# Kernel optimization log

Hardware: AMD Instinct MI355X
Metric: run time of the kernel (lower is better)

Reference implementation:

```python
import jax, jax.numpy as jnp
import numpy as np

NUM_ITER = 3
SLOT_DIM = 16
INPUT_DIM = 256
HIDDEN_DIM = 128
EPS = 1e-8
LN_EPS = 1e-5  # torch LayerNorm default


def _layernorm(x, w, b):
    mu = jnp.mean(x, axis=-1, keepdims=True)
    var = jnp.mean((x - mu) ** 2, axis=-1, keepdims=True)
    return (x - mu) * jax.lax.rsqrt(var + LN_EPS) * w + b


def setup_inputs() -> dict:
    key = jax.random.key(0)
    ks = jax.random.split(key, 12)
    B, N, K = 32, 4096, 8
    D, S, H = INPUT_DIM, SLOT_DIM, HIDDEN_DIM
    inputs = jax.random.normal(ks[0], (B, N, D), dtype=jnp.float32)
    init_slots = jax.random.normal(ks[1], (B, K, S), dtype=jnp.float32)
    return {
        "inputs": inputs,
        "init_slots": init_slots,
        "ln_in_w": jnp.ones((D,), jnp.float32),
        "ln_in_b": jnp.zeros((D,), jnp.float32),
        "ln_s_w": jnp.ones((S,), jnp.float32),
        "ln_s_b": jnp.zeros((S,), jnp.float32),
        "ln_m_w": jnp.ones((S,), jnp.float32),
        "ln_m_b": jnp.zeros((S,), jnp.float32),
        "wq": jax.random.normal(ks[2], (S, S), jnp.float32) * (S ** -0.5),
        "wk": jax.random.normal(ks[3], (S, D), jnp.float32) * (D ** -0.5),
        "wv": jax.random.normal(ks[4], (S, D), jnp.float32) * (D ** -0.5),
        "w_ih": jax.random.normal(ks[5], (3 * S, S), jnp.float32) * (S ** -0.5),
        "w_hh": jax.random.normal(ks[6], (3 * S, S), jnp.float32) * (S ** -0.5),
        "b_ih": jnp.zeros((3 * S,), jnp.float32),
        "b_hh": jnp.zeros((3 * S,), jnp.float32),
        "mlp_w1": jax.random.normal(ks[7], (H, S), jnp.float32) * (S ** -0.5),
        "mlp_b1": jnp.zeros((H,), jnp.float32),
        "mlp_w2": jax.random.normal(ks[8], (S, H), jnp.float32) * (H ** -0.5),
        "mlp_b2": jnp.zeros((S,), jnp.float32),
    }


def _gru_cell(x, h, w_ih, w_hh, b_ih, b_hh):
    # torch GRUCell: gates ordered [r, z, n]
    gi = x @ w_ih.T + b_ih            # [BK, 3S]
    gh = h @ w_hh.T + b_hh
    i_r, i_z, i_n = jnp.split(gi, 3, axis=-1)
    h_r, h_z, h_n = jnp.split(gh, 3, axis=-1)
    r = jax.nn.sigmoid(i_r + h_r)
    z = jax.nn.sigmoid(i_z + h_z)
    n = jnp.tanh(i_n + r * h_n)
    return (1.0 - z) * n + z * h


def reference(inputs, init_slots, ln_in_w, ln_in_b, ln_s_w, ln_s_b, ln_m_w, ln_m_b,
              wq, wk, wv, w_ih, w_hh, b_ih, b_hh, mlp_w1, mlp_b1, mlp_w2, mlp_b2):
    B, N, _ = inputs.shape
    K = init_slots.shape[1]
    scale = SLOT_DIM ** -0.5

    x = _layernorm(inputs, ln_in_w, ln_in_b)
    k = jnp.einsum('bnd,sd->bns', x, wk)   # [B,N,S]
    v = jnp.einsum('bnd,sd->bns', x, wv)

    slots = init_slots
    attn = None
    for _ in range(NUM_ITER):
        slots_prev = slots
        q = jnp.einsum('bks,ts->bkt', _layernorm(slots, ln_s_w, ln_s_b), wq)
        logits = jnp.einsum('bks,bns->bkn', q, k) * scale       # [B,K,N]
        attn = jax.nn.softmax(logits, axis=1) + EPS              # softmax over SLOTS
        attn = attn / jnp.sum(attn, axis=-1, keepdims=True)
        updates = jnp.einsum('bkn,bns->bks', attn, v)            # [B,K,S]
        h = _gru_cell(updates.reshape(B * K, -1), slots_prev.reshape(B * K, -1),
                      w_ih, w_hh, b_ih, b_hh).reshape(B, K, -1)
        y = _layernorm(h, ln_m_w, ln_m_b)
        mlp = jax.nn.relu(y @ mlp_w1.T + mlp_b1) @ mlp_w2.T + mlp_b2
        slots = h + mlp
    return slots, attn
```

## Files before the change

kernel.cpp:

```cpp
#include <hip/hip_runtime.h>
#include <cstddef>


__device__ __forceinline__ float sigmoid_f(float x){ return 1.f/(1.f+__expf(-x)); }
__device__ __forceinline__ float tanh_f(float x){ return 1.f - 2.f/(__expf(2.f*x)+1.f); }

__device__ __forceinline__ void load16_to_lds(const float* g, float* l) {
  __builtin_amdgcn_global_load_lds(
      (const __attribute__((address_space(1))) unsigned int*)g,
      (__attribute__((address_space(3))) unsigned int*)l,
      16, 0, 0);
}

__global__ __launch_bounds__(256) void k_prep(
    const float* __restrict__ lnw, const float* __restrict__ lnb,
    const float* __restrict__ wk, const float* __restrict__ wv,
    const float* __restrict__ init_slots,
    const float* __restrict__ ln_s_w, const float* __restrict__ ln_s_b,
    const float* __restrict__ wq,
    float* __restrict__ wprepT, float* __restrict__ mt,
    float* __restrict__ qbuf, float* __restrict__ upd, float* __restrict__ Abuf,
    float* __restrict__ slots_out)
{
  int t = threadIdx.x;
  int i = blockIdx.x*256 + t;
  {
    int d64 = i & 63, u = (i >> 6) & 7, p = (i >> 9) & 3, c = i >> 11;
    int s = p*8 + u, d = c*64 + d64;
    float w = (s < 16) ? wk[s*256+d] : wv[(s-16)*256+d];
    wprepT[i] = lnw[d]*w;
  }
  if (blockIdx.x != 0) return;
  {
    int s = t >> 3, j = t & 7;
    float m = 0.f, tv = 0.f;
    for (int d = j; d < 256; d += 8) {
      float w = (s < 16) ? wk[s*256+d] : wv[(s-16)*256+d];
      m  = fmaf(lnw[d], w, m);
      tv = fmaf(lnb[d], w, tv);
    }
    m += __shfl_xor(m,1);  m += __shfl_xor(m,2);  m += __shfl_xor(m,4);
    tv += __shfl_xor(tv,1); tv += __shfl_xor(tv,2); tv += __shfl_xor(tv,4);
    if (j == 0) { mt[s] = m; mt[32+s] = tv; }
  }
  #pragma unroll
  for (int j2 = 0; j2 < 16; ++j2) {
    slots_out[t*16+j2] = init_slots[t*16+j2];
    upd[t*16+j2] = 0.f;
  }
  Abuf[t] = 0.f;
  float sl[16];
  #pragma unroll
  for (int j2 = 0; j2 < 16; ++j2) sl[j2] = init_slots[t*16+j2];
  float mu = 0.f;
  #pragma unroll
  for (int j2 = 0; j2 < 16; ++j2) mu += sl[j2];
  mu *= (1.f/16.f);
  float var = 0.f;
  #pragma unroll
  for (int j2 = 0; j2 < 16; ++j2) { float d = sl[j2]-mu; var = fmaf(d,d,var); }
  var *= (1.f/16.f);
  float rstd = rsqrtf(var + 1e-5f);
  float y[16];
  #pragma unroll
  for (int j2 = 0; j2 < 16; ++j2) y[j2] = (sl[j2]-mu)*rstd*ln_s_w[j2] + ln_s_b[j2];
  #pragma unroll
  for (int tq = 0; tq < 16; ++tq) {
    float q = 0.f;
    #pragma unroll
    for (int s2 = 0; s2 < 16; ++s2) q = fmaf(y[s2], wq[tq*16+s2], q);
    qbuf[t*16+tq] = q;
  }
}

__global__ __launch_bounds__(256, 4) void k_proj(
    const float* __restrict__ x, const float* __restrict__ wprepT,
    const float* __restrict__ mt,
    float* __restrict__ kout, float* __restrict__ vout)
{
  __shared__ float xs[2][64*64];
  int t = threadIdx.x;
  int lane = t & 63;
  int p = __builtin_amdgcn_readfirstlane(t >> 6);
  int r0 = blockIdx.x*64;
  const float* xbase = x + (size_t)r0*256;

  int sr = lane >> 4;
  int slot = lane & 15;
  int row_st0 = p*16 + sr;
  int cb0 = (slot - row_st0) & 15;

  float acc[8];
  #pragma unroll
  for (int u = 0; u < 8; ++u) acc[u] = 0.f;
  float sum = 0.f, sumsq = 0.f;

  #define ISSUE_CHUNK(c_, buf_)                                              \
    _Pragma("unroll")                                                        \
    for (int i = 0; i < 4; ++i) {                                            \
      int row = row_st0 + i*4;                                               \
      int cb  = (cb0 - i*4) & 15;                                            \
      load16_to_lds(xbase + (size_t)row*256 + (c_)*64 + cb*4,                \
                    &xs[buf_][(p*16 + i*4)*64]);                             \
    }

  ISSUE_CHUNK(0, 0)
  __syncthreads();

  #pragma unroll 1
  for (int c = 0; c < 4; ++c) {
    if (c < 3) { ISSUE_CHUNK(c+1, (c+1)&1) }
    const float* wc = wprepT + (c*4 + p)*512;
    const float* xb = xs[c&1];
    #pragma unroll
    for (int g = 0; g < 4; ++g) {
      float xe[16];
      #pragma unroll
      for (int i = 0; i < 4; ++i) {
        int m = g*4 + i;
        float4 f = *(const float4*)&xb[lane*64 + ((m + lane) & 15)*4];
        xe[i*4+0]=f.x; xe[i*4+1]=f.y; xe[i*4+2]=f.z; xe[i*4+3]=f.w;
      }
      #pragma unroll
      for (int j = 0; j < 16; ++j) { sum += xe[j]; sumsq = fmaf(xe[j], xe[j], sumsq); }
      #pragma unroll
      for (int u = 0; u < 8; ++u) {
        const float* w = wc + u*64 + g*16;
        #pragma unroll
        for (int j = 0; j < 16; ++j) acc[u] = fmaf(xe[j], w[j], acc[u]);
      }
    }
    __syncthreads();
  }
  #undef ISSUE_CHUNK

  float mu = sum*(1.f/256.f);
  float var = sumsq*(1.f/256.f) - mu*mu;
  float rstd = rsqrtf(var + 1e-5f);
  float o[8];
  #pragma unroll
  for (int u = 0; u < 8; ++u) {
    int a = p*8 + u;
    o[u] = fmaf(rstd, acc[u] - mu*mt[a], mt[32+a]);
  }
  float* dst = ((p < 2) ? kout : vout) + (size_t)(r0 + lane)*16 + (p & 1)*8;
  *(float4*)(dst+0) = make_float4(o[0],o[1],o[2],o[3]);
  *(float4*)(dst+4) = make_float4(o[4],o[5],o[6],o[7]);
}

__global__ __launch_bounds__(256) void k_attn(
    const float* __restrict__ kproj, const float* __restrict__ vproj,
    const float* __restrict__ qbuf,
    float* __restrict__ upd, float* __restrict__ Abuf,
    float* __restrict__ attn_out, int write_attn)
{
  __shared__ float qs[128];
  __shared__ float ktile[256*20];
  __shared__ float vtile[16*260];
  __shared__ float ptile[8*260];
  int b = blockIdx.x >> 4;
  int n0 = (blockIdx.x & 15) * 256;
  int t = threadIdx.x;

  const float* kbase = kproj + ((size_t)(b*4096 + n0))*16;
  const float* vbase = vproj + ((size_t)(b*4096 + n0))*16;
  {
    int nn = t >> 2, s0 = (t & 3)*4;
    #pragma unroll
    for (int i = 0; i < 4; ++i) {
      int n = i*64 + nn;
      float4 kf = *(const float4*)(kbase + n*16 + s0);
      *(float4*)&ktile[n*20 + s0] = kf;
      float4 vf = *(const float4*)(vbase + n*16 + s0);
      vtile[(s0+0)*260 + n] = vf.x;
      vtile[(s0+1)*260 + n] = vf.y;
      vtile[(s0+2)*260 + n] = vf.z;
      vtile[(s0+3)*260 + n] = vf.w;
    }
  }
  if (t < 128) qs[t] = qbuf[b*128 + t];
  __syncthreads();

  {
    float4 kv[4];
    #pragma unroll
    for (int i = 0; i < 4; ++i) kv[i] = *(const float4*)&ktile[t*20 + i*4];
    const float4* q4 = (const float4*)qs;
    float lg[8];
    #pragma unroll
    for (int kk = 0; kk < 8; ++kk) {
      float4 a4 = make_float4(0.f,0.f,0.f,0.f);
      #pragma unroll
      for (int i = 0; i < 4; ++i) {
        float4 q = q4[kk*4+i];
        a4.x = fmaf(q.x, kv[i].x, a4.x);
        a4.y = fmaf(q.y, kv[i].y, a4.y);
        a4.z = fmaf(q.z, kv[i].z, a4.z);
        a4.w = fmaf(q.w, kv[i].w, a4.w);
      }
      lg[kk] = ((a4.x+a4.y)+(a4.z+a4.w))*0.25f;
    }
    float mx = lg[0];
    #pragma unroll
    for (int kk = 1; kk < 8; ++kk) mx = fmaxf(mx, lg[kk]);
    float se = 0.f;
    #pragma unroll
    for (int kk = 0; kk < 8; ++kk) { lg[kk] = __expf(lg[kk]-mx); se += lg[kk]; }
    float inv = 1.f/se;
    #pragma unroll
    for (int kk = 0; kk < 8; ++kk) {
      float pv = fmaf(lg[kk], inv, 1e-8f);
      ptile[kk*260 + t] = pv;
      if (write_attn) attn_out[((size_t)(b*8+kk))*4096 + n0 + t] = pv;
    }
  }
  __syncthreads();
  {
    int kk = t >> 5, r = t & 31, s = r >> 1, half = r & 1;
    const float4* pr = (const float4*)(ptile + kk*260 + half*128);
    const float4* vr = (const float4*)(vtile + s*260 + half*128);
    float4 a4 = make_float4(0.f,0.f,0.f,0.f);
    float4 s4 = make_float4(0.f,0.f,0.f,0.f);
    #pragma unroll 8
    for (int i = 0; i < 32; ++i) {
      float4 pv = pr[i], vv = vr[i];
      s4.x += pv.x; s4.y += pv.y; s4.z += pv.z; s4.w += pv.w;
      a4.x = fmaf(pv.x, vv.x, a4.x);
      a4.y = fmaf(pv.y, vv.y, a4.y);
      a4.z = fmaf(pv.z, vv.z, a4.z);
      a4.w = fmaf(pv.w, vv.w, a4.w);
    }
    float acc  = (a4.x+a4.y)+(a4.z+a4.w);
    float asum = (s4.x+s4.y)+(s4.z+s4.w);
    acc  += __shfl_xor(acc, 1);
    asum += __shfl_xor(asum, 1);
    if (half == 0) {
      atomicAdd(upd + (b*8+kk)*16 + s, acc);
      if (s == 0) atomicAdd(Abuf + b*8 + kk, asum);
    }
  }
}

__global__ __launch_bounds__(256) void k_gru(
    float* __restrict__ upd, float* __restrict__ Abuf,
    float* __restrict__ slots, float* __restrict__ qbuf,
    const float* __restrict__ w_ih, const float* __restrict__ w_hh,
    const float* __restrict__ b_ih, const float* __restrict__ b_hh,
    const float* __restrict__ mlp_w1, const float* __restrict__ mlp_b1,
    const float* __restrict__ mlp_w2, const float* __restrict__ mlp_b2,
    const float* __restrict__ ln_m_w, const float* __restrict__ ln_m_b,
    const float* __restrict__ ln_s_w, const float* __restrict__ ln_s_b,
    const float* __restrict__ wq, int prep_next)
{
  __shared__ float s_wih[48*17], s_whh[48*17];
  __shared__ float s_bih[48], s_bhh[48];
  __shared__ float s_w1[128*17], s_b1[128];
  __shared__ float s_w2[16*129], s_b2[16];
  __shared__ float s_lnmw[16], s_lnmb[16], s_lnsw[16], s_lnsb[16];
  __shared__ float s_wq[16*17];
  int t = threadIdx.x;
  for (int i = t; i < 768; i += 256) {
    int g = i >> 4, j = i & 15;
    s_wih[g*17+j] = w_ih[i];
    s_whh[g*17+j] = w_hh[i];
  }
  for (int i = t; i < 2048; i += 256) {
    int r = i >> 4, c = i & 15;
    s_w1[r*17+c] = mlp_w1[i];
    int r2 = i >> 7, c2 = i & 127;
    s_w2[r2*129+c2] = mlp_w2[i];
  }
  if (t < 48) { s_bih[t] = b_ih[t]; s_bhh[t] = b_hh[t]; }
  if (t < 128) s_b1[t] = mlp_b1[t];
  if (t < 16) {
    s_b2[t] = mlp_b2[t];
    s_lnmw[t] = ln_m_w[t]; s_lnmb[t] = ln_m_b[t];
    s_lnsw[t] = ln_s_w[t]; s_lnsb[t] = ln_s_b[t];
  }
  for (int i = t; i < 256; i += 256) {
    int r = i >> 4, c = i & 15;
    s_wq[r*17+c] = wq[i];
  }
  __syncthreads();

  int bk = blockIdx.x*16 + (t >> 4);
  int s = t & 15;
  int laneBase = (t & 63) & ~15;

  float inv = 1.f / Abuf[bk];
  float u[16], h[16];
  #pragma unroll
  for (int j = 0; j < 16; ++j) {
    u[j] = upd[bk*16+j] * inv;
    h[j] = slots[bk*16+j];
  }
  float hs = slots[bk*16+s];

  float gir = s_bih[s],  giz = s_bih[16+s], gin = s_bih[32+s];
  float ghr = s_bhh[s],  ghz = s_bhh[16+s], ghn = s_bhh[32+s];
  #pragma unroll
  for (int j = 0; j < 16; ++j) {
    gir = fmaf(u[j], s_wih[s*17+j], gir);
    giz = fmaf(u[j], s_wih[(16+s)*17+j], giz);
    gin = fmaf(u[j], s_wih[(32+s)*17+j], gin);
    ghr = fmaf(h[j], s_whh[s*17+j], ghr);
    ghz = fmaf(h[j], s_whh[(16+s)*17+j], ghz);
    ghn = fmaf(h[j], s_whh[(32+s)*17+j], ghn);
  }
  float rr = sigmoid_f(gir + ghr);
  float zz = sigmoid_f(giz + ghz);
  float nn = tanh_f(gin + rr*ghn);
  float hn = (1.f-zz)*nn + zz*hs;

  float ssum = hn;
  #pragma unroll
  for (int m = 1; m < 16; m <<= 1) ssum += __shfl_xor(ssum, m);
  float mu = ssum*(1.f/16.f);
  float dv = hn - mu;
  float vs = dv*dv;
  #pragma unroll
  for (int m = 1; m < 16; m <<= 1) vs += __shfl_xor(vs, m);
  float rstd = rsqrtf(vs*(1.f/16.f) + 1e-5f);
  float y = dv*rstd*s_lnmw[s] + s_lnmb[s];

  float yv[16];
  #pragma unroll
  for (int j = 0; j < 16; ++j) yv[j] = __shfl(y, laneBase + j);

  float h1[8];
  #pragma unroll
  for (int i = 0; i < 8; ++i) {
    int jj = i*16 + s;
    float a = s_b1[jj];
    #pragma unroll
    for (int q = 0; q < 16; ++q) a = fmaf(yv[q], s_w1[jj*17+q], a);
    h1[i] = fmaxf(a, 0.f);
  }
  float o = s_b2[s];
  #pragma unroll
  for (int i = 0; i < 8; ++i) {
    #pragma unroll
    for (int sp = 0; sp < 16; ++sp) {
      float hv = __shfl(h1[i], laneBase + sp);
      o = fmaf(hv, s_w2[s*129 + i*16 + sp], o);
    }
  }
  float slot_new = hn + o;
  slots[bk*16+s] = slot_new;

  if (prep_next) {
    float ss = slot_new;
    #pragma unroll
    for (int m = 1; m < 16; m <<= 1) ss += __shfl_xor(ss, m);
    float mu2 = ss*(1.f/16.f);
    float d2 = slot_new - mu2;
    float v2 = d2*d2;
    #pragma unroll
    for (int m = 1; m < 16; m <<= 1) v2 += __shfl_xor(v2, m);
    float rstd2 = rsqrtf(v2*(1.f/16.f) + 1e-5f);
    float y2 = d2*rstd2*s_lnsw[s] + s_lnsb[s];
    float qv = 0.f;
    #pragma unroll
    for (int sp = 0; sp < 16; ++sp) qv = fmaf(__shfl(y2, laneBase+sp), s_wq[s*17+sp], qv);
    qbuf[bk*16+s] = qv;
    upd[bk*16+s] = 0.f;
    if (s == 0) Abuf[bk] = 0.f;
  }
}

__global__ __launch_bounds__(256) void k_scale(float* __restrict__ attn,
                                               const float* __restrict__ Abuf)
{
  int bk = blockIdx.x;
  float inv = 1.f / Abuf[bk];
  float4* p = (float4*)(attn + (size_t)bk*4096);
  #pragma unroll 4
  for (int i = threadIdx.x; i < 1024; i += 256) {
    float4 v = p[i];
    v.x *= inv; v.y *= inv; v.z *= inv; v.w *= inv;
    p[i] = v;
  }
}

extern "C" void kernel_launch(void* const* d_in, const int* in_sizes, int n_in,
                              void* d_out, int out_size, void* d_ws, size_t ws_size,
                              hipStream_t stream)
{
  const float* inputs     = (const float*)d_in[0];
  const float* init_slots = (const float*)d_in[1];
  const float* ln_in_w    = (const float*)d_in[2];
  const float* ln_in_b    = (const float*)d_in[3];
  const float* ln_s_w     = (const float*)d_in[4];
  const float* ln_s_b     = (const float*)d_in[5];
  const float* ln_m_w     = (const float*)d_in[6];
  const float* ln_m_b     = (const float*)d_in[7];
  const float* wq         = (const float*)d_in[8];
  const float* wk         = (const float*)d_in[9];
  const float* wv         = (const float*)d_in[10];
  const float* w_ih       = (const float*)d_in[11];
  const float* w_hh       = (const float*)d_in[12];
  const float* b_ih       = (const float*)d_in[13];
  const float* b_hh       = (const float*)d_in[14];
  const float* mlp_w1     = (const float*)d_in[15];
  const float* mlp_b1     = (const float*)d_in[16];
  const float* mlp_w2     = (const float*)d_in[17];
  const float* mlp_b2     = (const float*)d_in[18];

  float* ws    = (float*)d_ws;
  float* wprepT= ws;
  float* mt    = ws + 8192;
  float* qbuf  = ws + 8320;
  float* upd   = ws + 12416;
  float* Abuf  = ws + 16512;
  float* kproj = ws + 16768;
  float* vproj = kproj + 2097152;

  float* out   = (float*)d_out;
  float* slots = out;
  float* attn  = out + 4096;

  k_prep<<<32, 256, 0, stream>>>(ln_in_w, ln_in_b, wk, wv, init_slots,
                                 ln_s_w, ln_s_b, wq,
                                 wprepT, mt, qbuf, upd, Abuf, slots);
  k_proj<<<2048, 256, 0, stream>>>(inputs, wprepT, mt, kproj, vproj);
  for (int it = 0; it < 3; ++it) {
    int last = (it == 2);
    k_attn<<<512, 256, 0, stream>>>(kproj, vproj, qbuf, upd, Abuf, attn, last);
    k_gru<<<16, 256, 0, stream>>>(upd, Abuf, slots, qbuf,
                                  w_ih, w_hh, b_ih, b_hh,
                                  mlp_w1, mlp_b1, mlp_w2, mlp_b2,
                                  ln_m_w, ln_m_b, ln_s_w, ln_s_b,
                                  wq, last ? 0 : 1);
  }
  k_scale<<<256, 256, 0, stream>>>(attn, Abuf);
}
```

Baseline: 338.1 us.

## Compute input K/V projection with split-bf16 MFMA instead of FP32 FMA

The K/V projection kernel now computes on bf16 matrix-core MFMA instructions, using a three-term hi/lo bf16 split of both inputs and weights to approximate FP32 accuracy. Weights are prepped as bf16 hi/lo pairs, and the layernorm mean correction term is adjusted to match the rounded weights. Inputs are read directly from global memory into registers, replacing the LDS double-buffering. This trades scalar FP32 FMA throughput for matrix-core throughput, at the cost of extra conversion work and a small precision loss.

```diff
diff --git a/kernel.cpp b/kernel.cpp
--- a/kernel.cpp
+++ b/kernel.cpp
@@ -2,14 +2,19 @@
 #include <cstddef>
 
 
+typedef unsigned short ushort_t;
+typedef __attribute__((ext_vector_type(8))) short short8;
+typedef __attribute__((ext_vector_type(4))) float f32x4;
+
 __device__ __forceinline__ float sigmoid_f(float x){ return 1.f/(1.f+__expf(-x)); }
 __device__ __forceinline__ float tanh_f(float x){ return 1.f - 2.f/(__expf(2.f*x)+1.f); }
 
-__device__ __forceinline__ void load16_to_lds(const float* g, float* l) {
-  __builtin_amdgcn_global_load_lds(
-      (const __attribute__((address_space(1))) unsigned int*)g,
-      (__attribute__((address_space(3))) unsigned int*)l,
-      16, 0, 0);
+__device__ __forceinline__ ushort_t f2bf(float x){
+  unsigned u = __float_as_uint(x);
+  return (ushort_t)((u + 0x7FFFu + ((u>>16)&1u)) >> 16);
+}
+__device__ __forceinline__ float bf2f(ushort_t b){
+  return __uint_as_float(((unsigned)b) << 16);
 }
 
 __global__ __launch_bounds__(256) void k_prep(
@@ -18,17 +23,20 @@
     const float* __restrict__ init_slots,
     const float* __restrict__ ln_s_w, const float* __restrict__ ln_s_b,
     const float* __restrict__ wq,
-    float* __restrict__ wprepT, float* __restrict__ mt,
+    ushort_t* __restrict__ Wh, ushort_t* __restrict__ Wl,
+    float* __restrict__ mt,
     float* __restrict__ qbuf, float* __restrict__ upd, float* __restrict__ Abuf,
     float* __restrict__ slots_out)
 {
   int t = threadIdx.x;
   int i = blockIdx.x*256 + t;
   {
-    int d64 = i & 63, u = (i >> 6) & 7, p = (i >> 9) & 3, c = i >> 11;
-    int s = p*8 + u, d = c*64 + d64;
+    int s = i >> 8, d = i & 255;
     float w = (s < 16) ? wk[s*256+d] : wv[(s-16)*256+d];
-    wprepT[i] = lnw[d]*w;
+    float w0 = lnw[d]*w;
+    ushort_t hb = f2bf(w0);
+    ushort_t lb = f2bf(w0 - bf2f(hb));
+    Wh[i] = hb; Wl[i] = lb;
   }
   if (blockIdx.x != 0) return;
   {
@@ -36,8 +44,12 @@
     float m = 0.f, tv = 0.f;
     for (int d = j; d < 256; d += 8) {
       float w = (s < 16) ? wk[s*256+d] : wv[(s-16)*256+d];
-      m  = fmaf(lnw[d], w, m);
-      tv = fmaf(lnb[d], w, tv);
+      float w0 = lnw[d]*w;
+      ushort_t hb = f2bf(w0);
+      float hf = bf2f(hb);
+      float lf = bf2f(f2bf(w0 - hf));
+      m  += hf + lf;
+      tv  = fmaf(lnb[d], w, tv);
     }
     m += __shfl_xor(m,1);  m += __shfl_xor(m,2);  m += __shfl_xor(m,4);
     tv += __shfl_xor(tv,1); tv += __shfl_xor(tv,2); tv += __shfl_xor(tv,4);
@@ -74,78 +86,67 @@
 }
 
 __global__ __launch_bounds__(256, 4) void k_proj(
-    const float* __restrict__ x, const float* __restrict__ wprepT,
-    const float* __restrict__ mt,
+    const float* __restrict__ x, const ushort_t* __restrict__ Wh,
+    const ushort_t* __restrict__ Wl, const float* __restrict__ mt,
     float* __restrict__ kout, float* __restrict__ vout)
 {
-  __shared__ float xs[2][64*64];
   int t = threadIdx.x;
-  int lane = t & 63;
-  int p = __builtin_amdgcn_readfirstlane(t >> 6);
-  int r0 = blockIdx.x*64;
-  const float* xbase = x + (size_t)r0*256;
-
-  int sr = lane >> 4;
-  int slot = lane & 15;
-  int row_st0 = p*16 + sr;
-  int cb0 = (slot - row_st0) & 15;
-
-  float acc[8];
-  #pragma unroll
-  for (int u = 0; u < 8; ++u) acc[u] = 0.f;
+  int w = t >> 6, lane = t & 63;
+  int m = lane & 15, quad = lane >> 4;
+  int r0w = blockIdx.x*64 + w*16;
+  const float* xr = x + (size_t)(r0w + m)*256 + quad*8;
+  const ushort_t* wh0 = Wh + (size_t)m*256 + quad*8;
+  const ushort_t* wh1 = wh0 + 16*256;
+  const ushort_t* wl0 = Wl + (size_t)m*256 + quad*8;
+  const ushort_t* wl1 = wl0 + 16*256;
+
+  f32x4 acck = {0.f,0.f,0.f,0.f}, accv = {0.f,0.f,0.f,0.f};
   float sum = 0.f, sumsq = 0.f;
 
-  #define ISSUE_CHUNK(c_, buf_)                                              \
-    _Pragma("unroll")                                                        \
-    for (int i = 0; i < 4; ++i) {                                            \
-      int row = row_st0 + i*4;                                               \
-      int cb  = (cb0 - i*4) & 15;                                            \
-      load16_to_lds(xbase + (size_t)row*256 + (c_)*64 + cb*4,                \
-                    &xs[buf_][(p*16 + i*4)*64]);                             \
-    }
-
-  ISSUE_CHUNK(0, 0)
-  __syncthreads();
-
-  #pragma unroll 1
-  for (int c = 0; c < 4; ++c) {
-    if (c < 3) { ISSUE_CHUNK(c+1, (c+1)&1) }
-    const float* wc = wprepT + (c*4 + p)*512;
-    const float* xb = xs[c&1];
-    #pragma unroll
-    for (int g = 0; g < 4; ++g) {
-      float xe[16];
-      #pragma unroll
-      for (int i = 0; i < 4; ++i) {
-        int m = g*4 + i;
-        float4 f = *(const float4*)&xb[lane*64 + ((m + lane) & 15)*4];
-        xe[i*4+0]=f.x; xe[i*4+1]=f.y; xe[i*4+2]=f.z; xe[i*4+3]=f.w;
-      }
-      #pragma unroll
-      for (int j = 0; j < 16; ++j) { sum += xe[j]; sumsq = fmaf(xe[j], xe[j], sumsq); }
-      #pragma unroll
-      for (int u = 0; u < 8; ++u) {
-        const float* w = wc + u*64 + g*16;
-        #pragma unroll
-        for (int j = 0; j < 16; ++j) acc[u] = fmaf(xe[j], w[j], acc[u]);
-      }
-    }
-    __syncthreads();
-  }
-  #undef ISSUE_CHUNK
-
-  float mu = sum*(1.f/256.f);
-  float var = sumsq*(1.f/256.f) - mu*mu;
-  float rstd = rsqrtf(var + 1e-5f);
-  float o[8];
-  #pragma unroll
-  for (int u = 0; u < 8; ++u) {
-    int a = p*8 + u;
-    o[u] = fmaf(rstd, acc[u] - mu*mt[a], mt[32+a]);
-  }
-  float* dst = ((p < 2) ? kout : vout) + (size_t)(r0 + lane)*16 + (p & 1)*8;
-  *(float4*)(dst+0) = make_float4(o[0],o[1],o[2],o[3]);
-  *(float4*)(dst+4) = make_float4(o[4],o[5],o[6],o[7]);
+  #pragma unroll
+  for (int kk = 0; kk < 8; ++kk) {
+    float4 a0 = *(const float4*)(xr + kk*32);
+    float4 a1 = *(const float4*)(xr + kk*32 + 4);
+    short8 bh_k = *(const short8*)(wh0 + kk*32);
+    short8 bh_v = *(const short8*)(wh1 + kk*32);
+    short8 bl_k = *(const short8*)(wl0 + kk*32);
+    short8 bl_v = *(const short8*)(wl1 + kk*32);
+    float xv[8] = {a0.x,a0.y,a0.z,a0.w, a1.x,a1.y,a1.z,a1.w};
+    short8 ah, al;
+    #pragma unroll
+    for (int j = 0; j < 8; ++j) {
+      float v = xv[j];
+      sum += v; sumsq = fmaf(v, v, sumsq);
+      ushort_t hb = f2bf(v);
+      ushort_t lb = f2bf(v - bf2f(hb));
+      ah[j] = (short)hb; al[j] = (short)lb;
+    }
+    acck = __builtin_amdgcn_mfma_f32_16x16x32_bf16(ah, bh_k, acck, 0, 0, 0);
+    accv = __builtin_amdgcn_mfma_f32_16x16x32_bf16(ah, bh_v, accv, 0, 0, 0);
+    acck = __builtin_amdgcn_mfma_f32_16x16x32_bf16(al, bh_k, acck, 0, 0, 0);
+    accv = __builtin_amdgcn_mfma_f32_16x16x32_bf16(al, bh_v, accv, 0, 0, 0);
+    acck = __builtin_amdgcn_mfma_f32_16x16x32_bf16(ah, bl_k, acck, 0, 0, 0);
+    accv = __builtin_amdgcn_mfma_f32_16x16x32_bf16(ah, bl_v, accv, 0, 0, 0);
+  }
+
+  sum   += __shfl_xor(sum, 16);  sum   += __shfl_xor(sum, 32);
+  sumsq += __shfl_xor(sumsq, 16); sumsq += __shfl_xor(sumsq, 32);
+
+  float mtk  = mt[m],    mtv  = mt[16+m];
+  float mtkb = mt[32+m], mtvb = mt[48+m];
+  #pragma unroll
+  for (int r = 0; r < 4; ++r) {
+    int row = quad*4 + r;
+    float s_ = __shfl(sum,   row);
+    float q_ = __shfl(sumsq, row);
+    float mu = s_*(1.f/256.f);
+    float var = q_*(1.f/256.f) - mu*mu;
+    float rstd = rsqrtf(var + 1e-5f);
+    float ok = fmaf(rstd, acck[r] - mu*mtk, mtkb);
+    float ov = fmaf(rstd, accv[r] - mu*mtv, mtvb);
+    kout[(size_t)(r0w + row)*16 + m] = ok;
+    vout[(size_t)(r0w + row)*16 + m] = ov;
+  }
 }
 
 __global__ __launch_bounds__(256) void k_attn(
@@ -407,7 +408,8 @@
   const float* mlp_b2     = (const float*)d_in[18];
 
   float* ws    = (float*)d_ws;
-  float* wprepT= ws;
+  ushort_t* Wh = (ushort_t*)ws;
+  ushort_t* Wl = (ushort_t*)(ws + 4096);
   float* mt    = ws + 8192;
   float* qbuf  = ws + 8320;
   float* upd   = ws + 12416;
@@ -421,8 +423,8 @@
 
   k_prep<<<32, 256, 0, stream>>>(ln_in_w, ln_in_b, wk, wv, init_slots,
                                  ln_s_w, ln_s_b, wq,
-                                 wprepT, mt, qbuf, upd, Abuf, slots);
-  k_proj<<<2048, 256, 0, stream>>>(inputs, wprepT, mt, kproj, vproj);
+                                 Wh, Wl, mt, qbuf, upd, Abuf, slots);
+  k_proj<<<2048, 256, 0, stream>>>(inputs, Wh, Wl, mt, kproj, vproj);
   for (int it = 0; it < 3; ++it) {
     int last = (it == 2);
     k_attn<<<512, 256, 0, stream>>>(kproj, vproj, qbuf, upd, Abuf, attn, last);
```

Result: faster. 302.9 us (-10.4%).
